# Optimization experiments

Measured on AMD Instinct MI355X. Metric: run time of the kernel, lower is better.

The kernel has to match this reference:

```python
import jax, jax.numpy as jnp
import numpy as np

N_HEADS = 16

def setup_inputs() -> dict:
    key = jax.random.key(0)
    ks = jax.random.split(key, 6)
    B, H, F, P, D = 2048, 1024, 4096, 512, 1024
    x = jax.random.normal(ks[0], (B, H), dtype=jnp.float32)
    # module inits features/prototypes ~ U(-0.27, 1)
    features = jax.random.uniform(ks[1], (F, D), minval=-0.27, maxval=1.0, dtype=jnp.float32)
    prototypes = jax.random.uniform(ks[2], (P, D), minval=-0.27, maxval=1.0, dtype=jnp.float32)
    # theta/alpha/beta are zero-init in the module; use small random values so output is non-trivial
    theta = jax.random.normal(ks[3], (N_HEADS, 1), dtype=jnp.float32)
    alpha = jax.random.normal(ks[4], (N_HEADS, 1), dtype=jnp.float32)
    beta = jax.random.normal(ks[5], (N_HEADS, 1), dtype=jnp.float32)
    return {"x": x, "features": features, "prototypes": prototypes,
            "theta": theta, "alpha": alpha, "beta": beta}

def reference(x, features, prototypes, theta, alpha, beta):
    n_heads = N_HEADS
    B, total_dim = x.shape
    d = total_dim // n_heads
    xh = x.reshape(B, n_heads, d)                       # b h d
    fh = features.reshape(-1, n_heads, d).transpose(1, 0, 2)    # h f d
    ph = prototypes.reshape(-1, n_heads, d).transpose(1, 0, 2)  # h p d
    x_features = jnp.einsum('bhd,hfd->bhf', xh, fh)     # [B,h,F]
    p_features = jnp.einsum('hpd,hfd->hpf', ph, fh)     # [h,P,F]
    x_present = jax.nn.relu(x_features)
    p_present = jax.nn.relu(p_features)
    x_weighted = x_features * x_present
    p_weighted = p_features * p_present
    # head-batched GEMMs sharing operands
    common = jnp.einsum('bhf,hpf->bhp', x_weighted, p_weighted)
    x_p_interaction = jnp.einsum('bhf,hpf->bhp', x_weighted, p_present)
    p_x_interaction = jnp.einsum('bhf,hpf->bhp', x_present, p_weighted)
    x_weighted_sum = x_weighted.sum(axis=2, keepdims=True)      # [B,h,1]
    p_weighted_sum = p_weighted.sum(axis=2)[None, :, :]         # [1,h,P]
    x_distinctive = x_weighted_sum - x_p_interaction
    p_distinctive = p_weighted_sum - p_x_interaction
    th = theta.reshape(1, n_heads, 1)
    al = alpha.reshape(1, n_heads, 1)
    be = beta.reshape(1, n_heads, 1)
    out = th * common - al * x_distinctive - be * p_distinctive  # [B,h,P]
    return out.reshape(B, -1)
```

## Files before the change

kernel.cpp:

```cpp
#include <hip/hip_runtime.h>
#include <cstdint>

#define NH 16
#define DH 64
#define FF 4096
#define PP 512
#define BB 2048

typedef __bf16 bf16x8 __attribute__((ext_vector_type(8)));
typedef float f32x4 __attribute__((ext_vector_type(4)));
typedef float f32x16 __attribute__((ext_vector_type(16)));
typedef float fl4 __attribute__((ext_vector_type(4)));
typedef unsigned short us4 __attribute__((ext_vector_type(4)));
typedef unsigned int u32x2 __attribute__((ext_vector_type(2)));

__device__ __forceinline__ unsigned short f2bf(float f) {
  unsigned u = __float_as_uint(f);
  u += 0x7FFFu + ((u >> 16) & 1u);
  return (unsigned short)(u >> 16);
}

__device__ __forceinline__ unsigned int pkbf(float lo, float hi) {
  unsigned a = __float_as_uint(lo) + 0x8000u;
  unsigned b = __float_as_uint(hi) + 0x8000u;
  return __builtin_amdgcn_perm(b, a, 0x07060302u);
}

__device__ __forceinline__ void gload_lds16(const void* g, void* l) {
  __builtin_amdgcn_global_load_lds(
      (const __attribute__((address_space(1))) void*)g,
      (__attribute__((address_space(3))) void*)(unsigned int)(unsigned long long)l,
      16, 0, 0);
}

__global__ void cvt_fp(const float* __restrict__ f, const float* __restrict__ p,
                       unsigned short* __restrict__ fb,
                       unsigned short* __restrict__ pb) {
  const int nf = FF * 1024 / 4, np = PP * 1024 / 4;
  int i = blockIdx.x * blockDim.x + threadIdx.x;
  const fl4* src;
  us4* dst;
  if (i < nf) {
    src = (const fl4*)f + i;
    dst = (us4*)fb + i;
  } else if (i < nf + np) {
    src = (const fl4*)p + (i - nf);
    dst = (us4*)pb + (i - nf);
  } else {
    return;
  }
  fl4 v = *src;
  us4 o;
  o.x = f2bf(v.x); o.y = f2bf(v.y); o.z = f2bf(v.z); o.w = f2bf(v.w);
  *dst = o;
}

__global__ __launch_bounds__(256, 2) void gemm_proto(
    const unsigned short* __restrict__ Abf, const unsigned short* __restrict__ Fbf,
    unsigned short* __restrict__ O1, unsigned short* __restrict__ O2,
    float* __restrict__ pws,
    const float* __restrict__ theta, const float* __restrict__ alpha,
    const float* __restrict__ beta) {
  const int h = blockIdx.z;
  const int n0 = blockIdx.x * 128;
  const int lm0 = blockIdx.y * 128;
  const int t = threadIdx.x;

  __shared__ __align__(16) char As[128 * 128];
  __shared__ __align__(16) char Bs[128 * 128];

  {
    const char* ab = (const char*)(Abf + (size_t)lm0 * 1024 + h * 64);
    const char* bb = (const char*)(Fbf + (size_t)n0 * 1024 + h * 64);
#pragma unroll
    for (int r = 0; r < 4; ++r) {
      int o = r * 4096 + t * 16;
      int row = o >> 7, col = o & 127;
      gload_lds16(ab + (size_t)row * 2048 + col, As + o);
      gload_lds16(bb + (size_t)row * 2048 + col, Bs + o);
    }
  }
  __syncthreads();

  const int wave = t >> 6, lane = t & 63;
  const int wm = wave & 1, wn = wave >> 1;
  const int quad = lane >> 4, lr = lane & 15;

  f32x4 acc[4][4];
#pragma unroll
  for (int i = 0; i < 4; ++i)
#pragma unroll
    for (int j = 0; j < 4; ++j) acc[i][j] = (f32x4){0.f, 0.f, 0.f, 0.f};

#pragma unroll
  for (int s = 0; s < 2; ++s) {
    bf16x8 av[4], bv[4];
#pragma unroll
    for (int fm = 0; fm < 4; ++fm) {
      int row = wm * 64 + fm * 16 + lr;
      av[fm] = *(const bf16x8*)(As + row * 128 + s * 64 + quad * 16);
    }
#pragma unroll
    for (int fn = 0; fn < 4; ++fn) {
      int row = wn * 64 + fn * 16 + lr;
      bv[fn] = *(const bf16x8*)(Bs + row * 128 + s * 64 + quad * 16);
    }
#pragma unroll
    for (int fm = 0; fm < 4; ++fm)
#pragma unroll
      for (int fn = 0; fn < 4; ++fn)
        acc[fm][fn] = __builtin_amdgcn_mfma_f32_16x16x32_bf16(av[fm], bv[fn],
                                                              acc[fm][fn], 0, 0, 0);
  }

  const float th = theta[h], al = alpha[h], be = beta[h];

#pragma unroll
  for (int fm = 0; fm < 4; ++fm) {
    int prow = lm0 + wm * 64 + fm * 16 + quad * 4;
    float rs0 = 0.f, rs1 = 0.f, rs2 = 0.f, rs3 = 0.f;
#pragma unroll
    for (int fn = 0; fn < 4; ++fn) {
      int f = n0 + wn * 64 + fn * 16 + lr;
#pragma unroll
      for (int i = 0; i < 4; ++i) {
        float pf = acc[fm][fn][i];
        float pp = fmaxf(pf, 0.f);
        float pw = pf * pp;
        size_t idx = ((size_t)(h * PP + prow + i)) * FF + f;
        O1[idx] = f2bf(th * pw + al * pp - al);
        O2[idx] = f2bf(be * pw);
        if (i == 0) rs0 += pw;
        else if (i == 1) rs1 += pw;
        else if (i == 2) rs2 += pw;
        else rs3 += pw;
      }
    }
    float rs[4] = {rs0, rs1, rs2, rs3};
#pragma unroll
    for (int i = 0; i < 4; ++i) {
      float s = rs[i];
      s += __shfl_xor(s, 1);
      s += __shfl_xor(s, 2);
      s += __shfl_xor(s, 4);
      s += __shfl_xor(s, 8);
      if (lr == 0) atomicAdd(&pws[h * PP + prow + i], be * s);
    }
  }
}

__global__ __launch_bounds__(256, 2) void fused_main(
    const float* __restrict__ x, const unsigned short* __restrict__ f_bf,
    const unsigned short* __restrict__ Q1, const unsigned short* __restrict__ Q2,
    const float* __restrict__ pws, float* __restrict__ out) {
  const int l = blockIdx.x;
  const int i = l >> 3;
  const int g = (l & 7) * 4 + (i & 3);
  const int h = g >> 1;
  const int n0 = (g & 1) * 256;
  const int m0 = (i >> 2) * 128;
  const int t = threadIdx.x;
  const int wave = t >> 6, lane = t & 63;
  const int quad = lane >> 4, lr = lane & 15;
  const int el = lane & 31, half = lane >> 5;
  const int key8 = lr & 7;
  const int key2 = (lr >> 1) & 3;

  __shared__ __align__(16) char sF[2 * 4096];
  __shared__ __align__(16) char sXw[2 * 8192];
  __shared__ __align__(16) char sXp[2 * 8192];

  bf16x8 xh[2][2];
#pragma unroll
  for (int bn = 0; bn < 2; ++bn)
#pragma unroll
    for (int s = 0; s < 2; ++s) {
      int b = m0 + wave * 32 + bn * 16 + lr;
      const float* xr = x + (size_t)b * 1024 + h * 64 + s * 32 + quad * 8;
      fl4 v0 = *(const fl4*)xr;
      fl4 v1 = *(const fl4*)(xr + 4);
      union { unsigned u[4]; bf16x8 v; } cv;
      cv.u[0] = pkbf(v0.x, v0.y);
      cv.u[1] = pkbf(v0.z, v0.w);
      cv.u[2] = pkbf(v1.x, v1.y);
      cv.u[3] = pkbf(v1.z, v1.w);
      xh[bn][s] = cv.v;
    }

  int af_off[2][2];
#pragma unroll
  for (int fm = 0; fm < 2; ++fm)
#pragma unroll
    for (int s = 0; s < 2; ++s)
      af_off[fm][s] = (fm * 16 + lr) * 128 + (((s * 4 + quad) ^ key8) * 16);

  int cw_off[2][2];
#pragma unroll
  for (int fm = 0; fm < 2; ++fm)
#pragma unroll
    for (int bn = 0; bn < 2; ++bn)
      cw_off[fm][bn] = (wave * 32 + bn * 16 + lr) * 64 +
                       (((fm * 2 + (quad >> 1)) ^ key2) * 16) + (quad & 1) * 8;

  int axk[2];
  {
    int keyel = ((el & 15) >> 1) & 3;
#pragma unroll
    for (int ks = 0; ks < 2; ++ks)
      axk[ks] = el * 64 + (((ks * 2 + half) ^ keyel) * 16);
  }

  const char* srcF;
  {
    int row = t >> 3, c = t & 7, cs = c ^ (row & 7);
    srcF = (const char*)f_bf + h * 128 + (size_t)row * 2048 + cs * 16;
  }

  const char* qb1 = (const char*)Q1 + (size_t)(h * PP + n0) * FF * 2;
  const char* qb2 = (const char*)Q2 + (size_t)(h * PP + n0) * FF * 2;
  unsigned qo = (unsigned)(((wave * 64 + el) * FF + half * 8) * 2);

  f32x16 acc[4][2];
#pragma unroll
  for (int mt = 0; mt < 4; ++mt)
#pragma unroll
    for (int nt = 0; nt < 2; ++nt)
#pragma unroll
      for (int r = 0; r < 16; ++r) acc[mt][nt][r] = 0.f;

  f32x4 xf[2][2];
  bf16x8 q1v[2][2], q2v[2][2];
  bf16x8 awf[2][2], apf[2][2];

#define BSTEP(SFB) do {                                                      \
    _Pragma("unroll") for (int fm_ = 0; fm_ < 2; ++fm_)                      \
      _Pragma("unroll") for (int bn_ = 0; bn_ < 2; ++bn_)                    \
        xf[fm_][bn_] = (f32x4){0.f, 0.f, 0.f, 0.f};                          \
    _Pragma("unroll") for (int s_ = 0; s_ < 2; ++s_)                         \
      _Pragma("unroll") for (int fm_ = 0; fm_ < 2; ++fm_) {                  \
        bf16x8 af_ = *(const bf16x8*)(sF + (SFB) + af_off[fm_][s_]);         \
        _Pragma("unroll") for (int bn_ = 0; bn_ < 2; ++bn_)                  \
          xf[fm_][bn_] = __builtin_amdgcn_mfma_f32_16x16x32_bf16(            \
              af_, xh[bn_][s_], xf[fm_][bn_], 0, 0, 0);                      \
      }                                                                      \
  } while (0)

#define CPACK(FM, BN, XB) do {                                               \
    float v0_ = xf[FM][BN][0], v1_ = xf[FM][BN][1];                          \
    float v2_ = xf[FM][BN][2], v3_ = xf[FM][BN][3];                          \
    float p0_ = fmaxf(v0_, 0.f), p1_ = fmaxf(v1_, 0.f);                      \
    float p2_ = fmaxf(v2_, 0.f), p3_ = fmaxf(v3_, 0.f);                      \
    u32x2 w_, p_;                                                            \
    w_.x = pkbf(v0_ * p0_, v1_ * p1_);                                       \
    w_.y = pkbf(v2_ * p2_, v3_ * p3_);                                       \
    p_.x = pkbf(p0_, p1_);                                                   \
    p_.y = pkbf(p2_, p3_);                                                   \
    *(u32x2*)(sXw + (XB) + cw_off[FM][BN]) = w_;                             \
    *(u32x2*)(sXp + (XB) + cw_off[FM][BN]) = p_;                             \
  } while (0)

#define DREAD32(P, XA) do {                                                  \
    _Pragma("unroll") for (int m_ = 0; m_ < 2; ++m_)                         \
      _Pragma("unroll") for (int ks_ = 0; ks_ < 2; ++ks_) {                  \
        awf[m_][ks_] =                                                       \
            *(const bf16x8*)(sXw + (XA) + (P) * 4096 + m_ * 2048 + axk[ks_]);\
        apf[m_][ks_] =                                                       \
            *(const bf16x8*)(sXp + (XA) + (P) * 4096 + m_ * 2048 + axk[ks_]);\
      }                                                                      \
  } while (0)

#define DM32(P, KS) do {                                                     \
    _Pragma("unroll") for (int m_ = 0; m_ < 2; ++m_)                         \
      _Pragma("unroll") for (int nt_ = 0; nt_ < 2; ++nt_) {                  \
        acc[(P) * 2 + m_][nt_] = __builtin_amdgcn_mfma_f32_32x32x16_bf16(    \
            awf[m_][KS], q1v[nt_][KS], acc[(P) * 2 + m_][nt_], 0, 0, 0);     \
        acc[(P) * 2 + m_][nt_] = __builtin_amdgcn_mfma_f32_32x32x16_bf16(    \
            apf[m_][KS], q2v[nt_][KS], acc[(P) * 2 + m_][nt_], 0, 0, 0);     \
      }                                                                      \
  } while (0)

#define QLOAD() do {                                                         \
    _Pragma("unroll") for (int nt_ = 0; nt_ < 2; ++nt_)                      \
      _Pragma("unroll") for (int ks_ = 0; ks_ < 2; ++ks_) {                  \
        q1v[nt_][ks_] =                                                      \
            *(const bf16x8*)(qb1 + qo + nt_ * 262144 + ks_ * 32);            \
        q2v[nt_][ks_] =                                                      \
            *(const bf16x8*)(qb2 + qo + nt_ * 262144 + ks_ * 32);            \
      }                                                                      \
  } while (0)

#define BODY(PA_, PB_) do {                                                  \
    gload_lds16(srcF, sF + (PA_) * 4096 + t * 16);                           \
    srcF += 32 * 2048;                                                       \
    BSTEP((PB_) * 4096);                                                     \
    DREAD32(0, (PA_) * 8192);                                                \
    __builtin_amdgcn_sched_barrier(0);                                       \
    __builtin_amdgcn_s_setprio(1);                                           \
    CPACK(0, 0, (PB_) * 8192);                                               \
    DM32(0, 0);                                                              \
    __builtin_amdgcn_sched_barrier(0);                                       \
    CPACK(0, 1, (PB_) * 8192);                                               \
    DM32(0, 1);                                                              \
    DREAD32(1, (PA_) * 8192);                                                \
    __builtin_amdgcn_sched_barrier(0);                                       \
    CPACK(1, 0, (PB_) * 8192);                                               \
    DM32(1, 0);                                                              \
    __builtin_amdgcn_sched_barrier(0);                                       \
    CPACK(1, 1, (PB_) * 8192);                                               \
    DM32(1, 1);                                                              \
    __builtin_amdgcn_s_setprio(0);                                           \
    QLOAD();                                                                 \
    qo += 64;                                                                \
      \
      \
      \
    asm volatile("s_waitcnt vmcnt(8) lgkmcnt(0)\n\ts_barrier" ::: "memory"); \
    __builtin_amdgcn_sched_barrier(0);                                       \
  } while (0)

  gload_lds16(srcF, sF + t * 16);
  srcF += 32 * 2048;
  asm volatile("s_waitcnt vmcnt(0)\n\ts_barrier" ::: "memory");
  __builtin_amdgcn_sched_barrier(0);
  gload_lds16(srcF, sF + 4096 + t * 16);
  srcF += 32 * 2048;
  BSTEP(0);
  CPACK(0, 0, 0);
  CPACK(0, 1, 0);
  CPACK(1, 0, 0);
  CPACK(1, 1, 0);
  QLOAD();
  qo += 64;
  asm volatile("s_waitcnt vmcnt(8) lgkmcnt(0)\n\ts_barrier" ::: "memory");
  __builtin_amdgcn_sched_barrier(0);

  for (int it2 = 0; it2 < FF / 64; ++it2) {
    BODY(0, 1);
    BODY(1, 0);
  }

#pragma unroll
  for (int nt = 0; nt < 2; ++nt) {
    int p = n0 + wave * 64 + nt * 32 + el;
    float sub = pws[h * PP + p];
#pragma unroll
    for (int mt = 0; mt < 4; ++mt) {
#pragma unroll
      for (int gi = 0; gi < 4; ++gi) {
#pragma unroll
        for (int r = 0; r < 4; ++r) {
          int b = m0 + mt * 32 + gi * 8 + half * 4 + r;
          out[(size_t)b * (NH * PP) + h * PP + p] = acc[mt][nt][gi * 4 + r] - sub;
        }
      }
    }
  }
}

extern "C" void kernel_launch(void* const* d_in, const int* in_sizes, int n_in,
                              void* d_out, int out_size, void* d_ws, size_t ws_size,
                              hipStream_t stream) {
  const float* x = (const float*)d_in[0];
  const float* features = (const float*)d_in[1];
  const float* prototypes = (const float*)d_in[2];
  const float* theta = (const float*)d_in[3];
  const float* alpha = (const float*)d_in[4];
  const float* beta = (const float*)d_in[5];
  float* out = (float*)d_out;

  char* ws = (char*)d_ws;
  size_t off = 0;
  auto carve = [&](size_t bytes) -> char* {
    char* p = ws + off;
    off += (bytes + 255) & ~(size_t)255;
    return p;
  };
  unsigned short* f_bf = (unsigned short*)carve((size_t)(FF + 64) * 1024 * 2);
  unsigned short* p_bf = (unsigned short*)carve((size_t)PP * 1024 * 2);
  unsigned short* Q1 = (unsigned short*)carve((size_t)NH * PP * FF * 2);
  unsigned short* Q2 = (unsigned short*)carve((size_t)NH * PP * FF * 2);
  float* pws = (float*)carve((size_t)NH * PP * 4);

  const int ncvt = (FF + PP) * 1024 / 4;
  cvt_fp<<<(ncvt + 255) / 256, 256, 0, stream>>>(features, prototypes, f_bf, p_bf);
  hipMemsetAsync(pws, 0, (size_t)NH * PP * 4, stream);

  gemm_proto<<<dim3(FF / 128, PP / 128, NH), 256, 0, stream>>>(
      p_bf, f_bf, Q1, Q2, pws, theta, alpha, beta);

  fused_main<<<dim3(512, 1, 1), 256, 0, stream>>>(
      x, f_bf, Q1, Q2, pws, out);
}
```

Baseline: 395.9 us.

## Shrink fused_main tile to 128x128 with 2x2 wave split for higher occupancy

The main fused kernel's per-block output tile shrinks from 128 batch rows by 256 prototypes to 128x128. Waves are now arranged 2x2 over batch and prototype instead of 4 along prototypes, which halves the accumulator registers per wave and allows three blocks per CU. The grid doubles to 1024 blocks with a new block-to-head mapping. The trade-off is that each block recomputes the x-feature GEMM and ReLU packing for half as many prototypes, doubling that redundant work, and Q operand reuse per block drops.

```diff
diff --git a/kernel.cpp b/kernel.cpp
--- a/kernel.cpp
+++ b/kernel.cpp
@@ -149,18 +149,19 @@
   }
 }
 
-__global__ __launch_bounds__(256, 2) void fused_main(
+__global__ __launch_bounds__(256, 3) void fused_main(
     const float* __restrict__ x, const unsigned short* __restrict__ f_bf,
     const unsigned short* __restrict__ Q1, const unsigned short* __restrict__ Q2,
     const float* __restrict__ pws, float* __restrict__ out) {
   const int l = blockIdx.x;
   const int i = l >> 3;
-  const int g = (l & 7) * 4 + (i & 3);
-  const int h = g >> 1;
-  const int n0 = (g & 1) * 256;
-  const int m0 = (i >> 2) * 128;
+  const int g = (l & 7) * 8 + (i >> 4);
+  const int h = g >> 2;
+  const int n0 = (g & 3) * 128;
+  const int m0 = (i & 15) * 128;
   const int t = threadIdx.x;
   const int wave = t >> 6, lane = t & 63;
+  const int wb = wave & 1, wp = wave >> 1;
   const int quad = lane >> 4, lr = lane & 15;
   const int el = lane & 31, half = lane >> 5;
   const int key8 = lr & 7;
@@ -218,11 +219,11 @@
 
   const char* qb1 = (const char*)Q1 + (size_t)(h * PP + n0) * FF * 2;
   const char* qb2 = (const char*)Q2 + (size_t)(h * PP + n0) * FF * 2;
-  unsigned qo = (unsigned)(((wave * 64 + el) * FF + half * 8) * 2);
-
-  f32x16 acc[4][2];
-#pragma unroll
-  for (int mt = 0; mt < 4; ++mt)
+  unsigned qo = (unsigned)(((wp * 64 + el) * FF + half * 8) * 2);
+
+  f32x16 acc[2][2];
+#pragma unroll
+  for (int mt = 0; mt < 2; ++mt)
 #pragma unroll
     for (int nt = 0; nt < 2; ++nt)
 #pragma unroll
@@ -259,24 +260,22 @@
     *(u32x2*)(sXp + (XB) + cw_off[FM][BN]) = p_;                             \
   } while (0)
 
-#define DREAD32(P, XA) do {                                                  \
-    _Pragma("unroll") for (int m_ = 0; m_ < 2; ++m_)                         \
-      _Pragma("unroll") for (int ks_ = 0; ks_ < 2; ++ks_) {                  \
-        awf[m_][ks_] =                                                       \
-            *(const bf16x8*)(sXw + (XA) + (P) * 4096 + m_ * 2048 + axk[ks_]);\
-        apf[m_][ks_] =                                                       \
-            *(const bf16x8*)(sXp + (XA) + (P) * 4096 + m_ * 2048 + axk[ks_]);\
-      }                                                                      \
-  } while (0)
-
-#define DM32(P, KS) do {                                                     \
-    _Pragma("unroll") for (int m_ = 0; m_ < 2; ++m_)                         \
-      _Pragma("unroll") for (int nt_ = 0; nt_ < 2; ++nt_) {                  \
-        acc[(P) * 2 + m_][nt_] = __builtin_amdgcn_mfma_f32_32x32x16_bf16(    \
-            awf[m_][KS], q1v[nt_][KS], acc[(P) * 2 + m_][nt_], 0, 0, 0);     \
-        acc[(P) * 2 + m_][nt_] = __builtin_amdgcn_mfma_f32_32x32x16_bf16(    \
-            apf[m_][KS], q2v[nt_][KS], acc[(P) * 2 + m_][nt_], 0, 0, 0);     \
-      }                                                                      \
+#define DREAD32(MT, XA) do {                                                 \
+    _Pragma("unroll") for (int ks_ = 0; ks_ < 2; ++ks_) {                    \
+      awf[MT][ks_] = *(const bf16x8*)(sXw + (XA) + wb * 4096 +               \
+                                      (MT) * 2048 + axk[ks_]);               \
+      apf[MT][ks_] = *(const bf16x8*)(sXp + (XA) + wb * 4096 +               \
+                                      (MT) * 2048 + axk[ks_]);               \
+    }                                                                        \
+  } while (0)
+
+#define DM32(MT, KS) do {                                                    \
+    _Pragma("unroll") for (int nt_ = 0; nt_ < 2; ++nt_) {                    \
+      acc[MT][nt_] = __builtin_amdgcn_mfma_f32_32x32x16_bf16(                \
+          awf[MT][KS], q1v[nt_][KS], acc[MT][nt_], 0, 0, 0);                 \
+      acc[MT][nt_] = __builtin_amdgcn_mfma_f32_32x32x16_bf16(                \
+          apf[MT][KS], q2v[nt_][KS], acc[MT][nt_], 0, 0, 0);                 \
+    }                                                                        \
   } while (0)
 
 #define QLOAD() do {                                                         \
@@ -341,15 +340,15 @@
 
 #pragma unroll
   for (int nt = 0; nt < 2; ++nt) {
-    int p = n0 + wave * 64 + nt * 32 + el;
+    int p = n0 + wp * 64 + nt * 32 + el;
     float sub = pws[h * PP + p];
 #pragma unroll
-    for (int mt = 0; mt < 4; ++mt) {
+    for (int mt = 0; mt < 2; ++mt) {
 #pragma unroll
       for (int gi = 0; gi < 4; ++gi) {
 #pragma unroll
         for (int r = 0; r < 4; ++r) {
-          int b = m0 + mt * 32 + gi * 8 + half * 4 + r;
+          int b = m0 + wb * 64 + mt * 32 + gi * 8 + half * 4 + r;
           out[(size_t)b * (NH * PP) + h * PP + p] = acc[mt][nt][gi * 4 + r] - sub;
         }
       }
@@ -388,6 +387,6 @@
   gemm_proto<<<dim3(FF / 128, PP / 128, NH), 256, 0, stream>>>(
       p_bf, f_bf, Q1, Q2, pws, theta, alpha, beta);
 
-  fused_main<<<dim3(512, 1, 1), 256, 0, stream>>>(
+  fused_main<<<dim3(1024, 1, 1), 256, 0, stream>>>(
       x, f_bf, Q1, Q2, pws, out);
 }
```

Result: slower. 726.1 us (+83.4%).
